# Kernel tuning notes

Hardware: AMD Instinct MI355X
Metric: run time of the kernel (lower is better)

The kernel has to match this reference:

```python
import jax, jax.numpy as jnp
import numpy as np

H = 128          # hidden_channels
K = 3            # TAGConv hops
NV, NS = 100000, 50000
EVV, ESS, EH, EIN = 1_000_000, 500_000, 500_000, 300_000


def setup_inputs() -> dict:
    key = jax.random.key(0)
    ks = iter(jax.random.split(key, 40))
    def rn(shape, s=0.05):
        return jax.random.normal(next(ks), shape, jnp.float32) * s
    def ri(shape, hi):
        return jax.random.randint(next(ks), shape, 0, hi, jnp.int32)
    return {
        "game_x": rn((NV, 5), 1.0),
        "state_x": rn((NS, 6), 1.0),
        "edge_index_v_v": ri((2, EVV), NV),
        "edge_type_v_v": ri((EVV,), 4),  # unused in forward (interface fidelity)
        "edge_index_history_v_s": jnp.stack([ri((EH,), NV), ri((EH,), NS)]),
        "edge_attr_history_v_s": rn((EH, 1), 1.0),
        "edge_index_in_v_s": jnp.stack([ri((EIN,), NV), ri((EIN,), NS)]),
        "edge_index_s_s": ri((2, ESS), NS),
        # TAGConv weights: (K+1) hop linears, shared bias
        "tag1_W": rn((K + 1, 5, H)), "tag1_b": rn((H,)),
        "tag2_W": rn((K + 1, 6, H)), "tag2_b": rn((H,)),
        # 7 SAGEConv layers stacked: gv[1:3]=0,1; sv[1:3]=2,3; in1=4; sv2=5,6
        "sage_Wl": rn((7, H, H)), "sage_bl": rn((7, H)), "sage_Wr": rn((7, H, H)),
        # GATConv (1 head, edge_dim=1)
        "gat_Wsrc": rn((H, H)), "gat_Wdst": rn((H, H)), "gat_We": rn((1, H)),
        "gat_asrc": rn((H,)), "gat_adst": rn((H,)), "gat_ae": rn((H,)), "gat_b": rn((H,)),
        # final MLP: single Linear(H, 1)
        "mlp_W": rn((H, 1)), "mlp_b": rn((1,)),
    }


def _seg_sum(x, idx, n):
    return jax.ops.segment_sum(x, idx, num_segments=n)


def tag_conv(x, edge_index, n, W, b):
    """TAGConv: out = sum_k lin_k(A_norm^k x) + b, gcn_norm w/o self loops."""
    src, dst = edge_index[0], edge_index[1]
    deg = _seg_sum(jnp.ones(src.shape, x.dtype), dst, n)
    dinv = jnp.where(deg > 0, jax.lax.rsqrt(jnp.maximum(deg, 1.0)), 0.0)
    norm = dinv[src] * dinv[dst]                      # [E]
    out = x @ W[0]
    h = x
    for k in range(1, W.shape[0]):
        h = _seg_sum(h[src] * norm[:, None], dst, n)  # one hop of normalized A
        out = out + h @ W[k]
    return out + b


def sage_conv(x_src, x_dst, edge_index, n_dst, Wl, bl, Wr):
    """SAGEConv(mean): lin_l(mean_j x_src[j]) + lin_r(x_dst)."""
    src, dst = edge_index[0], edge_index[1]
    s = _seg_sum(x_src[src], dst, n_dst)
    cnt = _seg_sum(jnp.ones(src.shape, x_src.dtype), dst, n_dst)
    mean = s / jnp.maximum(cnt, 1.0)[:, None]
    return mean @ Wl + bl + x_dst @ Wr


def gat_conv(x_src, x_dst, edge_index, edge_attr, n_dst,
             Wsrc, Wdst, We, asrc, adst, ae, b):
    """Bipartite GATConv, 1 head, edge features, no self loops."""
    src, dst = edge_index[0], edge_index[1]
    hs = x_src @ Wsrc                                  # [NV, H]
    hd = x_dst @ Wdst                                  # [NS, H]
    a = (hs @ asrc)[src] + (hd @ adst)[dst] + (edge_attr @ We) @ ae  # [E]
    a = jax.nn.leaky_relu(a, 0.2)
    m = jax.ops.segment_max(a, dst, num_segments=n_dst)
    e = jnp.exp(a - m[dst])                            # segment softmax
    denom = _seg_sum(e, dst, n_dst)
    alpha = e / jnp.maximum(denom, 1e-16)[dst]
    out = _seg_sum(alpha[:, None] * hs[src], dst, n_dst)
    return out + b


def reference(game_x, state_x, edge_index_v_v, edge_type_v_v,
              edge_index_history_v_s, edge_attr_history_v_s,
              edge_index_in_v_s, edge_index_s_s,
              tag1_W, tag1_b, tag2_W, tag2_b,
              sage_Wl, sage_bl, sage_Wr,
              gat_Wsrc, gat_Wdst, gat_We, gat_asrc, gat_adst, gat_ae, gat_b,
              mlp_W, mlp_b):
    relu = jax.nn.relu
    nv, ns = game_x.shape[0], state_x.shape[0]
    # game-vertex tower
    gx = relu(tag_conv(game_x, edge_index_v_v, nv, tag1_W, tag1_b))
    for i in range(2):
        gx = relu(sage_conv(gx, gx, edge_index_v_v, nv, sage_Wl[i], sage_bl[i], sage_Wr[i]))
    # state-vertex tower
    sx = relu(tag_conv(state_x, edge_index_s_s, ns, tag2_W, tag2_b))
    for i in range(2, 4):
        sx = relu(sage_conv(sx, sx, edge_index_s_s, ns, sage_Wl[i], sage_bl[i], sage_Wr[i]))
    # bipartite attention game -> state
    hist = relu(gat_conv(gx, sx, edge_index_history_v_s, edge_attr_history_v_s, ns,
                         gat_Wsrc, gat_Wdst, gat_We, gat_asrc, gat_adst, gat_ae, gat_b))
    in_x = relu(sage_conv(gx, hist, edge_index_in_v_s, ns, sage_Wl[4], sage_bl[4], sage_Wr[4]))
    # second state tower
    sx = in_x
    for i in range(5, 7):
        sx = relu(sage_conv(sx, sx, edge_index_s_s, ns, sage_Wl[i], sage_bl[i], sage_Wr[i]))
    return sx @ mlp_W + mlp_b                          # [NS, 1]
```

## Files before the change

### kernel.cpp

```cpp
#include <hip/hip_runtime.h>

#define H 128
typedef unsigned short u16;
typedef __attribute__((ext_vector_type(8))) short bf16x8;
typedef __attribute__((ext_vector_type(4))) float f32x4;


static inline int gridFor(long long work, int block, int cap = 16384){
  long long g = (work + block - 1) / block;
  if (g > cap) g = cap;
  if (g < 1) g = 1;
  return (int)g;
}

__device__ __forceinline__ float waveReduceSum(float v){
  #pragma unroll
  for(int off = 32; off > 0; off >>= 1) v += __shfl_down(v, off);
  return v;
}

__device__ __forceinline__ float bflo(unsigned v){ return __uint_as_float(v << 16); }
__device__ __forceinline__ float bfhi(unsigned v){ return __uint_as_float(v & 0xffff0000u); }
__device__ __forceinline__ u16 f2bf(float f){
  unsigned u = __float_as_uint(f);
  return (u16)((u + 0x7fffu + ((u >> 16) & 1u)) >> 16);
}
__device__ __forceinline__ unsigned pack2(float lo, float hi){
  return (unsigned)f2bf(lo) | ((unsigned)f2bf(hi) << 16);
}

#define BSHIFT 9
#define CH 2048

template<bool HAS_ATTR>
__global__ __launch_bounds__(256) void part_kernel(
    const int* __restrict__ src, const int* __restrict__ dst,
    const float* __restrict__ attr, int* __restrict__ bcur,
    int2* __restrict__ bpairs, float* __restrict__ battr, int E, int cap){
  __shared__ int hist[256];
  __shared__ int hscan[256];
  __shared__ int hbase[256];
  __shared__ int hcur[256];
  __shared__ int2 buf[CH];
  __shared__ float abuf[HAS_ATTR ? CH : 1];

  const int t = threadIdx.x;
  const int e0 = blockIdx.x * CH;
  const int cnt = min(CH, E - e0);

  hist[t] = 0; hcur[t] = 0;
  __syncthreads();

  #pragma unroll
  for(int j = 0; j < 8; j++){
    int i = e0 + j*256 + t;
    if(i - e0 < cnt) atomicAdd(&hist[dst[i] >> BSHIFT], 1);
  }
  __syncthreads();

  {
    int v = hist[t];
    int lane = t & 63, wid = t >> 6;
    int incl = v;
    #pragma unroll
    for(int off = 1; off < 64; off <<= 1){
      int u = __shfl_up(incl, off);
      if(lane >= off) incl += u;
    }
    __shared__ int ws4[4];
    if(lane == 63) ws4[wid] = incl;
    __syncthreads();
    int wofs = 0;
    for(int wj = 0; wj < wid; wj++) wofs += ws4[wj];
    hscan[t] = wofs + incl - v;
    hbase[t] = (v > 0) ? atomicAdd(&bcur[t], v) : 0;
  }
  __syncthreads();

  #pragma unroll
  for(int j = 0; j < 8; j++){
    int i = e0 + j*256 + t;
    if(i - e0 < cnt){
      int d = dst[i], s = src[i];
      int b = d >> BSHIFT;
      int lp = atomicAdd(&hcur[b], 1);
      int slot = hscan[b] + lp;
      buf[slot] = make_int2(d, s);
      if(HAS_ATTR) abuf[slot] = attr[i];
    }
  }
  __syncthreads();

  for(int u = t; u < cnt; u += 256){
    int2 pr = buf[u];
    int b = pr.x >> BSHIFT;
    int g = b * cap + hbase[b] + (u - hscan[b]);
    bpairs[g] = pr;
    if(HAS_ATTR) battr[g] = abuf[u];
  }
}

__global__ void bucket_scan(const int* __restrict__ bcur, int* __restrict__ bbase,
                            int* __restrict__ rp0, int* __restrict__ rp1,
                            int* __restrict__ rp2, int* __restrict__ rp3,
                            int n0, int n1, int n2, int n3){
  int g = blockIdx.x;
  int n = (g == 0) ? n0 : (g == 1) ? n1 : (g == 2) ? n2 : n3;
  int* rowp = (g == 0) ? rp0 : (g == 1) ? rp1 : (g == 2) ? rp2 : rp3;
  int NB = (n + 511) >> BSHIFT;
  int t = threadIdx.x;
  int v = (t < NB) ? bcur[g*256 + t] : 0;
  int lane = t & 63, wid = t >> 6;
  int incl = v;
  #pragma unroll
  for(int off = 1; off < 64; off <<= 1){
    int u = __shfl_up(incl, off);
    if(lane >= off) incl += u;
  }
  __shared__ int ws4[4];
  if(lane == 63) ws4[wid] = incl;
  __syncthreads();
  int wofs = 0;
  for(int wj = 0; wj < wid; wj++) wofs += ws4[wj];
  bbase[g*256 + t] = wofs + incl - v;
  if(t == 0) rowp[n] = ws4[0] + ws4[1] + ws4[2] + ws4[3];
}

template<bool HAS_ATTR, bool DINV>
__global__ __launch_bounds__(256) void build_kernel(
    const int2* __restrict__ bpairs, const float* __restrict__ battr,
    const int* __restrict__ bcur, const int* __restrict__ bbase,
    int* __restrict__ rowp, int* __restrict__ col, float* __restrict__ attrp,
    float* __restrict__ dinv, int cap, int n){
  __shared__ int hist[512];
  __shared__ int hcur[512];
  __shared__ int ws4[4];

  const int b = blockIdx.x;
  const int t = threadIdx.x;
  const int d0 = b << BSHIFT;
  const int dn = min(512, n - d0);
  const int cnt = bcur[b];
  const int base = bbase[b];
  const int2* ep = bpairs + (size_t)b * cap;

  hist[t] = 0; hist[t + 256] = 0;
  __syncthreads();
  for(int u = t; u < cnt; u += 256) atomicAdd(&hist[ep[u].x - d0], 1);
  __syncthreads();

  int a0 = hist[2*t], a1 = hist[2*t + 1];
  int s = a0 + a1;
  int lane = t & 63, wid = t >> 6;
  int incl = s;
  #pragma unroll
  for(int off = 1; off < 64; off <<= 1){
    int u = __shfl_up(incl, off);
    if(lane >= off) incl += u;
  }
  if(lane == 63) ws4[wid] = incl;
  __syncthreads();
  int wofs = 0;
  for(int wj = 0; wj < wid; wj++) wofs += ws4[wj];
  int excl = wofs + incl - s;
  __syncthreads();
  hcur[2*t] = excl; hcur[2*t + 1] = excl + a0;
  if(2*t < dn){
    rowp[d0 + 2*t] = base + excl;
    if(DINV) dinv[d0 + 2*t] = a0 > 0 ? rsqrtf((float)a0) : 0.f;
  }
  if(2*t + 1 < dn){
    rowp[d0 + 2*t + 1] = base + excl + a0;
    if(DINV) dinv[d0 + 2*t + 1] = a1 > 0 ? rsqrtf((float)a1) : 0.f;
  }
  __syncthreads();

  for(int u = t; u < cnt; u += 256){
    int2 pr = ep[u];
    int pos = base + atomicAdd(&hcur[pr.x - d0], 1);
    col[pos] = pr.y;
    if(HAS_ATTR) attrp[pos] = battr[(size_t)b * cap + u];
  }
}


__global__ void cvt_weights(const float* __restrict__ Wl, const float* __restrict__ Wr,
                            const float* __restrict__ Wsrc, u16* __restrict__ Wb){
  const int total = 15 * H * H;
  for(int t = blockIdx.x*blockDim.x + threadIdx.x; t < total; t += gridDim.x*blockDim.x){
    int mat = t >> 14, idx = t & 16383;
    int k = idx >> 7, colj = idx & 127;
    const float* srcp = (mat < 7) ? (Wl + ((size_t)mat << 14))
                       : (mat < 14) ? (Wr + ((size_t)(mat - 7) << 14))
                       : Wsrc;
    Wb[((size_t)mat << 14) + (size_t)colj*H + k] = f2bf(srcp[idx]);
  }
}

__global__ void mat_vec_row(const float* __restrict__ W, const float* __restrict__ a,
                            float* __restrict__ outv){
  int k = threadIdx.x;
  if(k < H){
    float s = 0.f;
    for(int j = 0; j < H; j++) s += W[(size_t)k*H + j] * a[j];
    outv[k] = s;
  }
}

__global__ void dot128(const float* __restrict__ a, const float* __restrict__ b,
                       float* __restrict__ o){
  int l = threadIdx.x;
  float acc = a[l]*b[l] + a[l+64]*b[l+64];
  acc = waveReduceSum(acc);
  if(l == 0) o[0] = acc;
}


template<int C>
__global__ void pack_rows(const float* __restrict__ x, const float* __restrict__ dinv,
                          float* __restrict__ xp, int N){
  for(int i = blockIdx.x*blockDim.x + threadIdx.x; i < N; i += gridDim.x*blockDim.x){
    #pragma unroll
    for(int k = 0; k < C; k++) xp[(size_t)i*8 + k] = x[(size_t)i*C + k];
    xp[(size_t)i*8 + 7] = dinv[i];
  }
}

template<int C>
__global__ void csr_tag_hop8(const int* __restrict__ rowp, const int* __restrict__ col,
                             const float* __restrict__ hin, float* __restrict__ hout, int N){
  for(int i = blockIdx.x*blockDim.x + threadIdx.x; i < N; i += gridDim.x*blockDim.x){
    int b = rowp[i], e = rowp[i+1];
    float dd = hin[(size_t)i*8 + 7];
    float acc0[C], acc1[C];
    #pragma unroll
    for(int k = 0; k < C; k++){ acc0[k] = 0.f; acc1[k] = 0.f; }
    int p = b;
    for(; p + 2 <= e; p += 2){
      const float* r0 = &hin[(size_t)col[p]   * 8];
      const float* r1 = &hin[(size_t)col[p+1] * 8];
      float w0 = r0[7] * dd, w1 = r1[7] * dd;
      #pragma unroll
      for(int k = 0; k < C; k++){
        acc0[k] += r0[k] * w0;
        acc1[k] += r1[k] * w1;
      }
    }
    if(p < e){
      const float* r0 = &hin[(size_t)col[p] * 8];
      float w0 = r0[7] * dd;
      #pragma unroll
      for(int k = 0; k < C; k++) acc0[k] += r0[k] * w0;
    }
    #pragma unroll
    for(int k = 0; k < C; k++) hout[(size_t)i*8 + k] = acc0[k] + acc1[k];
    hout[(size_t)i*8 + 7] = dd;
  }
}

template<int C>
__global__ __launch_bounds__(256) void tag_fuse(
    const float* __restrict__ x, const float* __restrict__ h1,
    const float* __restrict__ h2, const float* __restrict__ h3,
    const float* __restrict__ W, const float* __restrict__ bias,
    u16* __restrict__ out, int N){
  __shared__ float Ws[4*C*H];
  for(int u = threadIdx.x; u < 4*C*H; u += 256) Ws[u] = W[u];
  __syncthreads();
  const long long total = (long long)N * H;
  for(long long t = (long long)blockIdx.x*blockDim.x + threadIdx.x; t < total;
      t += (long long)gridDim.x*blockDim.x){
    int i = (int)(t >> 7), j = (int)(t & 127);
    const float* xr = x + (size_t)i*C;
    const float* r1 = h1 + (size_t)i*8;
    const float* r2 = h2 + (size_t)i*8;
    const float* r3 = h3 + (size_t)i*8;
    float acc = bias[j];
    #pragma unroll
    for(int k = 0; k < C; k++) acc += xr[k] * Ws[k*H + j];
    #pragma unroll
    for(int k = 0; k < C; k++) acc += r1[k] * Ws[(C + k)*H + j];
    #pragma unroll
    for(int k = 0; k < C; k++) acc += r2[k] * Ws[(2*C + k)*H + j];
    #pragma unroll
    for(int k = 0; k < C; k++) acc += r3[k] * Ws[(3*C + k)*H + j];
    out[t] = f2bf(fmaxf(acc, 0.f));
  }
}


__global__ __launch_bounds__(256) void sage_fused(
    const u16* __restrict__ G, const u16* __restrict__ X,
    const int* __restrict__ rowp, const int* __restrict__ col,
    const u16* __restrict__ WbR, const u16* __restrict__ WbL,
    const float* __restrict__ bl, u16* __restrict__ out, int N){
  __shared__ u16 Ws[H * H];

  const int t = threadIdx.x;
  const int lane = t & 63;
  const int wib = t >> 6;
  const int m0 = (blockIdx.x * 4 + wib) * 16;
  const int r16 = lane & 15;
  const int kg  = (lane >> 4) * 8;
  const bool active = (m0 < N);
  const int row = m0 + r16;

  for(int u = t; u < H*H/8; u += 256){
    bf16x8 v = *(const bf16x8*)&WbR[u*8];
    int c = u >> 4, kb = (u & 15) * 16;
    *(bf16x8*)((char*)Ws + c*256 + (kb ^ ((c & 7) << 4))) = v;
  }
  __syncthreads();

  f32x4 acc[8];
  #pragma unroll
  for(int tt = 0; tt < 8; tt++) acc[tt] = (f32x4){0.f,0.f,0.f,0.f};

  if(active){
    #pragma unroll
    for(int k0c = 0; k0c < 4; k0c++){
      int k0 = k0c * 32;
      bf16x8 af;
      if(row < N) af = *(const bf16x8*)&X[(size_t)row*H + k0 + kg];
      else        af = (bf16x8){0,0,0,0,0,0,0,0};
      #pragma unroll
      for(int tt = 0; tt < 8; tt++){
        int c = tt*16 + r16;
        int kb = (k0 + kg)*2;
        bf16x8 bf = *(const bf16x8*)((char*)Ws + c*256 + (kb ^ ((c & 7) << 4)));
        acc[tt] = __builtin_amdgcn_mfma_f32_16x16x32_bf16(af, bf, acc[tt], 0, 0, 0);
      }
    }
  }
  __syncthreads();

  for(int u = t; u < H*H/8; u += 256){
    bf16x8 v = *(const bf16x8*)&WbL[u*8];
    int c = u >> 4, kb = (u & 15) * 16;
    *(bf16x8*)((char*)Ws + c*256 + (kb ^ ((c & 7) << 4))) = v;
  }
  __syncthreads();

  if(active){
    float ag[4][8];
    #pragma unroll
    for(int kc = 0; kc < 4; kc++)
      #pragma unroll
      for(int j = 0; j < 8; j++) ag[kc][j] = 0.f;

    if(row < N){
      int b = rowp[row], e = rowp[row+1];
      for(int p = b; p < e; p++){
        int s = col[p];
        const u16* gr = &G[(size_t)s*H + kg];
        #pragma unroll
        for(int kc = 0; kc < 4; kc++){
          bf16x8 v = *(const bf16x8*)(gr + kc*32);
          const unsigned* vu = (const unsigned*)&v;
          #pragma unroll
          for(int q = 0; q < 4; q++){
            ag[kc][2*q]   += bflo(vu[q]);
            ag[kc][2*q+1] += bfhi(vu[q]);
          }
        }
      }
      float inv = 1.f / fmaxf((float)(e - b), 1.f);
      #pragma unroll
      for(int kc = 0; kc < 4; kc++)
        #pragma unroll
        for(int j = 0; j < 8; j++) ag[kc][j] *= inv;
    }

    #pragma unroll
    for(int kc = 0; kc < 4; kc++){
      unsigned uu[4];
      #pragma unroll
      for(int q = 0; q < 4; q++) uu[q] = pack2(ag[kc][2*q], ag[kc][2*q+1]);
      bf16x8 agb = *(bf16x8*)uu;
      int kb = (kc*32 + kg)*2;
      #pragma unroll
      for(int tt = 0; tt < 8; tt++){
        int c = tt*16 + r16;
        bf16x8 bf = *(const bf16x8*)((char*)Ws + c*256 + (kb ^ ((c & 7) << 4)));
        acc[tt] = __builtin_amdgcn_mfma_f32_16x16x32_bf16(agb, bf, acc[tt], 0, 0, 0);
      }
    }

    const int orow = m0 + (lane >> 4) * 4;
    #pragma unroll
    for(int tt = 0; tt < 8; tt++){
      int c = tt*16 + r16;
      float bb = bl[c];
      #pragma unroll
      for(int r = 0; r < 4; r++){
        if(orow + r < N){
          float v = fmaxf(acc[tt][r] + bb, 0.f);
          out[(size_t)(orow + r)*H + c] = f2bf(v);
        }
      }
    }
  }
}


__global__ __launch_bounds__(256) void gemm_mfma(
    const u16* __restrict__ x, const u16* __restrict__ Wb,
    u16* __restrict__ out, int N){
  __shared__ u16 Ws[H * H];
  const int t = threadIdx.x;
  for(int u = t; u < H*H/8; u += 256){
    bf16x8 v = *(const bf16x8*)&Wb[u*8];
    int c = u >> 4, kb = (u & 15) * 16;
    *(bf16x8*)((char*)Ws + c*256 + (kb ^ ((c & 7) << 4))) = v;
  }
  __syncthreads();

  const int lane = t & 63;
  const int wib = t >> 6;
  const int m0 = (blockIdx.x * 4 + wib) * 32;
  if(m0 >= N) return;
  const int r16 = lane & 15;
  const int kg = (lane >> 4) * 8;

  f32x4 acc[2][8];
  #pragma unroll
  for(int rt = 0; rt < 2; rt++)
    #pragma unroll
    for(int tt = 0; tt < 8; tt++) acc[rt][tt] = (f32x4){0.f,0.f,0.f,0.f};

  #pragma unroll
  for(int k0c = 0; k0c < 4; k0c++){
    int k0 = k0c * 32;
    bf16x8 af[2];
    #pragma unroll
    for(int rt = 0; rt < 2; rt++){
      int row = m0 + rt*16 + r16;
      if(row < N) af[rt] = *(const bf16x8*)&x[(size_t)row*H + k0 + kg];
      else        af[rt] = (bf16x8){0,0,0,0,0,0,0,0};
    }
    #pragma unroll
    for(int tt = 0; tt < 8; tt++){
      int c = tt*16 + r16;
      int kb = (k0 + kg)*2;
      bf16x8 bf = *(const bf16x8*)((char*)Ws + c*256 + (kb ^ ((c & 7) << 4)));
      acc[0][tt] = __builtin_amdgcn_mfma_f32_16x16x32_bf16(af[0], bf, acc[0][tt], 0, 0, 0);
      acc[1][tt] = __builtin_amdgcn_mfma_f32_16x16x32_bf16(af[1], bf, acc[1][tt], 0, 0, 0);
    }
  }

  #pragma unroll
  for(int rt = 0; rt < 2; rt++){
    const int orow = m0 + rt*16 + (lane >> 4) * 4;
    #pragma unroll
    for(int tt = 0; tt < 8; tt++){
      int c = tt*16 + r16;
      #pragma unroll
      for(int r = 0; r < 4; r++){
        if(orow + r < N)
          out[(size_t)(orow + r)*H + c] = f2bf(acc[rt][tt][r]);
      }
    }
  }
}


__global__ void rowdot_bf(const u16* __restrict__ x, const float* __restrict__ v,
                          float* __restrict__ out, int N){
  int lane = threadIdx.x & 63;
  int w = (blockIdx.x*blockDim.x + threadIdx.x) >> 6;
  int nw = (gridDim.x*blockDim.x) >> 6;
  for(int i = w; i < N; i += nw){
    unsigned u = *(const unsigned*)&x[(size_t)i*H + lane*2];
    float acc = bflo(u)*v[lane*2] + bfhi(u)*v[lane*2 + 1];
    acc = waveReduceSum(acc);
    if(lane == 0) out[i] = acc;
  }
}

__global__ void gat_fused(const int* __restrict__ rowp, const int* __restrict__ colv,
                          const float* __restrict__ attrp, const float* __restrict__ av,
                          const float* __restrict__ ad, const float* __restrict__ cptr,
                          const u16* __restrict__ hs, const float* __restrict__ bias,
                          u16* __restrict__ out, int N){
  const float c = cptr[0];
  int lane = threadIdx.x & 63;
  int w = (blockIdx.x*blockDim.x + threadIdx.x) >> 6;
  int nw = (gridDim.x*blockDim.x) >> 6;
  for(int i = w; i < N; i += nw){
    int b = rowp[i], e = rowp[i+1];
    float adi = ad[i];
    float accx0 = 0.f, accy0 = 0.f, accx1 = 0.f, accy1 = 0.f;
    float sume = 0.f;
    int p = b;
    for(; p + 2 <= e; p += 2){
      int s0 = colv[p], s1 = colv[p+1];
      float a0 = av[s0] + adi + attrp[p] * c;
      float a1 = av[s1] + adi + attrp[p+1] * c;
      a0 = a0 > 0.f ? a0 : 0.2f * a0;
      a1 = a1 > 0.f ? a1 : 0.2f * a1;
      float e0 = __expf(a0), e1 = __expf(a1);
      unsigned v0 = *(const unsigned*)&hs[(size_t)s0*H + lane*2];
      unsigned v1 = *(const unsigned*)&hs[(size_t)s1*H + lane*2];
      accx0 += e0 * bflo(v0); accy0 += e0 * bfhi(v0);
      accx1 += e1 * bflo(v1); accy1 += e1 * bfhi(v1);
      sume += e0 + e1;
    }
    if(p < e){
      int s0 = colv[p];
      float a0 = av[s0] + adi + attrp[p] * c;
      a0 = a0 > 0.f ? a0 : 0.2f * a0;
      float e0 = __expf(a0);
      unsigned v0 = *(const unsigned*)&hs[(size_t)s0*H + lane*2];
      accx0 += e0 * bflo(v0); accy0 += e0 * bfhi(v0);
      sume += e0;
    }
    float rd = 1.f / fmaxf(sume, 1e-16f);
    float ox = fmaxf((accx0 + accx1) * rd + bias[lane*2],     0.f);
    float oy = fmaxf((accy0 + accy1) * rd + bias[lane*2 + 1], 0.f);
    *(unsigned*)&out[(size_t)i*H + lane*2] = pack2(ox, oy);
  }
}

__global__ void mlp_out_bf(const u16* __restrict__ x, const float* __restrict__ W,
                           const float* __restrict__ b, float* __restrict__ out, int N){
  int lane = threadIdx.x & 63;
  int w = (blockIdx.x*blockDim.x + threadIdx.x) >> 6;
  int nw = (gridDim.x*blockDim.x) >> 6;
  for(int i = w; i < N; i += nw){
    unsigned u = *(const unsigned*)&x[(size_t)i*H + lane*2];
    float acc = bflo(u)*W[lane*2] + bfhi(u)*W[lane*2 + 1];
    acc = waveReduceSum(acc);
    if(lane == 0) out[i] = acc + b[0];
  }
}


extern "C" void kernel_launch(void* const* d_in, const int* in_sizes, int n_in,
                              void* d_out, int out_size, void* d_ws, size_t ws_size,
                              hipStream_t stream) {
  const float* game_x  = (const float*)d_in[0];
  const float* state_x = (const float*)d_in[1];
  const int*   e_vv    = (const int*)d_in[2];
  const int*   e_hist  = (const int*)d_in[4];
  const float* attr_h  = (const float*)d_in[5];
  const int*   e_in    = (const int*)d_in[6];
  const int*   e_ss    = (const int*)d_in[7];
  const float* tag1_W  = (const float*)d_in[8];
  const float* tag1_b  = (const float*)d_in[9];
  const float* tag2_W  = (const float*)d_in[10];
  const float* tag2_b  = (const float*)d_in[11];
  const float* sage_Wl = (const float*)d_in[12];
  const float* sage_bl = (const float*)d_in[13];
  const float* sage_Wr = (const float*)d_in[14];
  const float* gat_Wsrc= (const float*)d_in[15];
  const float* gat_Wdst= (const float*)d_in[16];
  const float* gat_We  = (const float*)d_in[17];
  const float* gat_asrc= (const float*)d_in[18];
  const float* gat_adst= (const float*)d_in[19];
  const float* gat_ae  = (const float*)d_in[20];
  const float* gat_b   = (const float*)d_in[21];
  const float* mlp_W   = (const float*)d_in[22];
  const float* mlp_b   = (const float*)d_in[23];
  float* out = (float*)d_out;

  const int NV  = in_sizes[0] / 5;
  const int NS  = in_sizes[1] / 6;
  const int EVV = in_sizes[2] / 2;
  const int EH  = in_sizes[4] / 2;
  const int EIN = in_sizes[6] / 2;
  const int ESS = in_sizes[7] / 2;

  const int* vv_src = e_vv;   const int* vv_dst = e_vv + EVV;
  const int* eh_src = e_hist; const int* eh_dst = e_hist + EH;
  const int* in_src = e_in;   const int* in_dst = e_in + EIN;
  const int* ss_src = e_ss;   const int* ss_dst = e_ss + ESS;

  const int NBv = (NV + 511) >> BSHIFT;
  const int NBs = (NS + 511) >> BSHIFT;
  const int capvv = (EVV / NBv) * 3 / 2 + 64;
  const int capss = (ESS / NBs) * 3 / 2 + 64;
  const int capeh = (EH  / NBs) * 3 / 2 + 64;
  const int capin = (EIN / NBs) * 3 / 2 + 64;

  char* wp = (char*)d_ws;
  auto alloc = [&](size_t bytes) -> void* {
    void* p = (void*)wp;
    wp += (bytes + 511) & ~size_t(511);
    return p;
  };
  u16* V0 = (u16*)alloc((size_t)NV*H*2);
  u16* V1 = (u16*)alloc((size_t)NV*H*2);
  u16* S0 = (u16*)alloc((size_t)NS*H*2);
  u16* S1 = (u16*)alloc((size_t)NS*H*2);
  u16* Wb = (u16*)alloc((size_t)15*H*H*2);
  float* dinv_v = (float*)alloc((size_t)NV*4);
  float* dinv_s = (float*)alloc((size_t)NS*4);
  float* av   = (float*)alloc((size_t)NV*4);
  float* ad   = (float*)alloc((size_t)NS*4);
  float* xp5  = (float*)alloc((size_t)NV*8*4);
  float* h5a  = (float*)alloc((size_t)NV*8*4);
  float* h5b  = (float*)alloc((size_t)NV*8*4);
  float* h5c  = (float*)alloc((size_t)NV*8*4);
  float* xp6  = (float*)alloc((size_t)NS*8*4);
  float* h6a  = (float*)alloc((size_t)NS*8*4);
  float* h6b  = (float*)alloc((size_t)NS*8*4);
  float* h6c  = (float*)alloc((size_t)NS*8*4);
  float* wvec = (float*)alloc(H*4);
  float* cbuf = (float*)alloc(4);
  int* vv_rowp = (int*)alloc((size_t)(NV+1)*4);
  int* vv_col  = (int*)alloc((size_t)EVV*4);
  int* ss_rowp = (int*)alloc((size_t)(NS+1)*4);
  int* ss_col  = (int*)alloc((size_t)ESS*4);
  int* eh_rowp = (int*)alloc((size_t)(NS+1)*4);
  int* eh_col  = (int*)alloc((size_t)EH*4);
  float* eh_attr = (float*)alloc((size_t)EH*4);
  int* in_rowp = (int*)alloc((size_t)(NS+1)*4);
  int* in_col  = (int*)alloc((size_t)EIN*4);
  int2* vv_bp = (int2*)alloc((size_t)NBv*capvv*8);
  int2* ss_bp = (int2*)alloc((size_t)NBs*capss*8);
  int2* eh_bp = (int2*)alloc((size_t)NBs*capeh*8);
  int2* in_bp = (int2*)alloc((size_t)NBs*capin*8);
  float* eh_ba = (float*)alloc((size_t)NBs*capeh*4);
  int* bcur  = (int*)alloc(4*256*4);
  int* bbase = (int*)alloc(4*256*4);
  (void)ws_size; (void)n_in; (void)out_size;

  const int B = 256;
  #define GRID1(n) gridFor((long long)(n), B, 8192), B, 0, stream
  #define GRIDW(e) gridFor((long long)(e) * 64, B, 16384), B, 0, stream
  #define GEMM(n)  ((n) + 63) / 64, 256, 0, stream

  hipMemsetAsync(bcur, 0, 4*256*4, stream);
  part_kernel<false><<<(EVV + CH - 1)/CH, 256, 0, stream>>>(
      vv_src, vv_dst, nullptr, bcur + 0,   vv_bp, nullptr, EVV, capvv);
  part_kernel<false><<<(ESS + CH - 1)/CH, 256, 0, stream>>>(
      ss_src, ss_dst, nullptr, bcur + 256, ss_bp, nullptr, ESS, capss);
  part_kernel<true ><<<(EH  + CH - 1)/CH, 256, 0, stream>>>(
      eh_src, eh_dst, attr_h,  bcur + 512, eh_bp, eh_ba,   EH,  capeh);
  part_kernel<false><<<(EIN + CH - 1)/CH, 256, 0, stream>>>(
      in_src, in_dst, nullptr, bcur + 768, in_bp, nullptr, EIN, capin);
  bucket_scan<<<4, 256, 0, stream>>>(bcur, bbase, vv_rowp, ss_rowp, eh_rowp, in_rowp,
                                     NV, NS, NS, NS);
  build_kernel<false,true ><<<NBv, 256, 0, stream>>>(
      vv_bp, nullptr, bcur + 0,   bbase + 0,   vv_rowp, vv_col, nullptr, dinv_v, capvv, NV);
  build_kernel<false,true ><<<NBs, 256, 0, stream>>>(
      ss_bp, nullptr, bcur + 256, bbase + 256, ss_rowp, ss_col, nullptr, dinv_s, capss, NS);
  build_kernel<true ,false><<<NBs, 256, 0, stream>>>(
      eh_bp, eh_ba,   bcur + 512, bbase + 512, eh_rowp, eh_col, eh_attr, nullptr, capeh, NS);
  build_kernel<false,false><<<NBs, 256, 0, stream>>>(
      in_bp, nullptr, bcur + 768, bbase + 768, in_rowp, in_col, nullptr, nullptr, capin, NS);

  cvt_weights<<<GRID1(15*H*H)>>>(sage_Wl, sage_Wr, gat_Wsrc, Wb);
  mat_vec_row<<<1, 128, 0, stream>>>(gat_Wdst, gat_adst, wvec);
  dot128<<<1, 64, 0, stream>>>(gat_We, gat_ae, cbuf);

  #define WBL(l) (Wb + ((size_t)(l) << 14))
  #define WBR(l) (Wb + ((size_t)(7 + (l)) << 14))

  pack_rows<5><<<GRID1(NV)>>>(game_x, dinv_v, xp5, NV);
  csr_tag_hop8<5><<<GRID1(NV)>>>(vv_rowp, vv_col, xp5, h5a, NV);
  csr_tag_hop8<5><<<GRID1(NV)>>>(vv_rowp, vv_col, h5a, h5b, NV);
  csr_tag_hop8<5><<<GRID1(NV)>>>(vv_rowp, vv_col, h5b, h5c, NV);
  tag_fuse<5><<<GRID1((long long)NV*H)>>>(game_x, h5a, h5b, h5c, tag1_W, tag1_b, V0, NV);

  sage_fused<<<GEMM(NV)>>>(V0, V0, vv_rowp, vv_col, WBR(0), WBL(0),
                           sage_bl + 0*H, V1, NV);
  sage_fused<<<GEMM(NV)>>>(V1, V1, vv_rowp, vv_col, WBR(1), WBL(1),
                           sage_bl + 1*H, V0, NV);

  pack_rows<6><<<GRID1(NS)>>>(state_x, dinv_s, xp6, NS);
  csr_tag_hop8<6><<<GRID1(NS)>>>(ss_rowp, ss_col, xp6, h6a, NS);
  csr_tag_hop8<6><<<GRID1(NS)>>>(ss_rowp, ss_col, h6a, h6b, NS);
  csr_tag_hop8<6><<<GRID1(NS)>>>(ss_rowp, ss_col, h6b, h6c, NS);
  tag_fuse<6><<<GRID1((long long)NS*H)>>>(state_x, h6a, h6b, h6c, tag2_W, tag2_b, S0, NS);

  sage_fused<<<GEMM(NS)>>>(S0, S0, ss_rowp, ss_col, WBR(2), WBL(2),
                           sage_bl + 2*H, S1, NS);
  sage_fused<<<GEMM(NS)>>>(S1, S1, ss_rowp, ss_col, WBR(3), WBL(3),
                           sage_bl + 3*H, S0, NS);

  gemm_mfma<<<((NV + 127)/128), 256, 0, stream>>>(V0, Wb + ((size_t)14 << 14), V1, NV);
  rowdot_bf<<<GRIDW(NV)>>>(V1, gat_asrc, av, NV);
  rowdot_bf<<<GRIDW(NS)>>>(S0, wvec, ad, NS);
  gat_fused<<<GRIDW(NS)>>>(eh_rowp, eh_col, eh_attr, av, ad, cbuf, V1, gat_b, S1, NS);

  sage_fused<<<GEMM(NS)>>>(V0, S1, in_rowp, in_col, WBR(4), WBL(4),
                           sage_bl + 4*H, S0, NS);

  sage_fused<<<GEMM(NS)>>>(S0, S0, ss_rowp, ss_col, WBR(5), WBL(5),
                           sage_bl + 5*H, S1, NS);
  sage_fused<<<GEMM(NS)>>>(S1, S1, ss_rowp, ss_col, WBR(6), WBL(6),
                           sage_bl + 6*H, S0, NS);

  mlp_out_bf<<<GRIDW(NS)>>>(S0, mlp_W, mlp_b, out, NS);

  #undef GRID1
  #undef GRIDW
  #undef GEMM
  #undef WBL
  #undef WBR
}
```

Baseline: 908.8 us.

## Gather SAGE neighbor rows wave-cooperatively per row and transpose via LDS

The mean-aggregation gather in the fused SAGE kernel changes from each lane walking one row's neighbor list with 16-byte loads to the whole wave processing one destination row at a time. Each lane loads 4 bytes of each neighbor row, giving coalesced 256-byte row reads, and the inner loop is unrolled 8 neighbors deep to keep more loads in flight. The results are staged in a small LDS buffer and read back in the MFMA A-fragment layout. This removes load imbalance from uneven degrees across the 16 rows in a wave, at the cost of serializing the 16 rows and extra LDS traffic.

```diff
diff --git a/kernel.cpp b/kernel.cpp
--- a/kernel.cpp
+++ b/kernel.cpp
@@ -295,6 +295,7 @@
     const u16* __restrict__ WbR, const u16* __restrict__ WbL,
     const float* __restrict__ bl, u16* __restrict__ out, int N){
   __shared__ u16 Ws[H * H];
+  __shared__ unsigned Tr[4][16][68];
 
   const int t = threadIdx.x;
   const int lane = t & 63;
@@ -303,7 +304,6 @@
   const int r16 = lane & 15;
   const int kg  = (lane >> 4) * 8;
   const bool active = (m0 < N);
-  const int row = m0 + r16;
 
   for(int u = t; u < H*H/8; u += 256){
     bf16x8 v = *(const bf16x8*)&WbR[u*8];
@@ -317,6 +317,7 @@
   for(int tt = 0; tt < 8; tt++) acc[tt] = (f32x4){0.f,0.f,0.f,0.f};
 
   if(active){
+    const int row = m0 + r16;
     #pragma unroll
     for(int k0c = 0; k0c < 4; k0c++){
       int k0 = k0c * 32;
@@ -342,41 +343,38 @@
   __syncthreads();
 
   if(active){
-    float ag[4][8];
-    #pragma unroll
-    for(int kc = 0; kc < 4; kc++)
-      #pragma unroll
-      for(int j = 0; j < 8; j++) ag[kc][j] = 0.f;
-
-    if(row < N){
-      int b = rowp[row], e = rowp[row+1];
-      for(int p = b; p < e; p++){
-        int s = col[p];
-        const u16* gr = &G[(size_t)s*H + kg];
+    for(int r = 0; r < 16; r++){
+      int row = m0 + r;
+      unsigned packed = 0;
+      if(row < N){
+        int b = rowp[row], e = rowp[row+1];
+        float xs[8], ys[8];
         #pragma unroll
-        for(int kc = 0; kc < 4; kc++){
-          bf16x8 v = *(const bf16x8*)(gr + kc*32);
-          const unsigned* vu = (const unsigned*)&v;
+        for(int j = 0; j < 8; j++){ xs[j] = 0.f; ys[j] = 0.f; }
+        int p = b;
+        for(; p + 8 <= e; p += 8){
+          unsigned v[8];
           #pragma unroll
-          for(int q = 0; q < 4; q++){
-            ag[kc][2*q]   += bflo(vu[q]);
-            ag[kc][2*q+1] += bfhi(vu[q]);
-          }
+          for(int j = 0; j < 8; j++)
+            v[j] = *(const unsigned*)&G[(size_t)col[p + j]*H + lane*2];
+          #pragma unroll
+          for(int j = 0; j < 8; j++){ xs[j] += bflo(v[j]); ys[j] += bfhi(v[j]); }
         }
+        for(; p < e; p++){
+          unsigned v = *(const unsigned*)&G[(size_t)col[p]*H + lane*2];
+          xs[0] += bflo(v); ys[0] += bfhi(v);
+        }
+        float sx = (xs[0]+xs[1])+(xs[2]+xs[3])+((xs[4]+xs[5])+(xs[6]+xs[7]));
+        float sy = (ys[0]+ys[1])+(ys[2]+ys[3])+((ys[4]+ys[5])+(ys[6]+ys[7]));
+        float inv = 1.f / fmaxf((float)(e - b), 1.f);
+        packed = pack2(sx*inv, sy*inv);
       }
-      float inv = 1.f / fmaxf((float)(e - b), 1.f);
-      #pragma unroll
-      for(int kc = 0; kc < 4; kc++)
-        #pragma unroll
-        for(int j = 0; j < 8; j++) ag[kc][j] *= inv;
+      Tr[wib][r][lane] = packed;
     }
 
     #pragma unroll
     for(int kc = 0; kc < 4; kc++){
-      unsigned uu[4];
-      #pragma unroll
-      for(int q = 0; q < 4; q++) uu[q] = pack2(ag[kc][2*q], ag[kc][2*q+1]);
-      bf16x8 agb = *(bf16x8*)uu;
+      bf16x8 agb = *(const bf16x8*)&Tr[wib][r16][(lane >> 4)*4 + kc*16];
       int kb = (kc*32 + kg)*2;
       #pragma unroll
       for(int tt = 0; tt < 8; tt++){
```

Measured after the change: 1.323 ms. 45.6% more time.

## Group SAGE rows by in-degree via permutation to balance wave gather loops

Applied to the files above, without the earlier changes.

Adds a deg_scatter kernel that builds, per graph, a permutation of destination rows bucketed by in-degree (capped at 63). Each 4096-row chunk groups its rows by degree and claims positions with a global atomic, so rows of equal degree sit together only inside a chunk. sage_fused now processes rows in permuted order, so the 16 rows in a wave have similar neighbour counts and less lane divergence in the gather loop. It also unrolls the neighbour loop by two to keep more loads in flight. The cost is scattered output writes and X reads, and extra indirection through perm.

```diff
diff --git a/kernel.cpp b/kernel.cpp
--- a/kernel.cpp
+++ b/kernel.cpp
@@ -183,6 +183,32 @@
   }
 }
 
+__global__ __launch_bounds__(256) void deg_scatter(
+    const int* __restrict__ rowp, int* __restrict__ gcur,
+    int* __restrict__ perm, int n){
+  __shared__ int lh[64], lbase[64], lcur[64];
+  const int t = threadIdx.x;
+  const int base = blockIdx.x * 4096;
+  if(base >= n) return;
+  const int cnt = min(4096, n - base);
+  if(t < 64){ lh[t] = 0; lcur[t] = 0; }
+  __syncthreads();
+  for(int i = t; i < cnt; i += 256){
+    int r = base + i;
+    int d = min(rowp[r+1] - rowp[r], 63);
+    atomicAdd(&lh[d], 1);
+  }
+  __syncthreads();
+  if(t < 64) lbase[t] = (lh[t] > 0) ? atomicAdd(gcur, lh[t]) : 0;
+  __syncthreads();
+  for(int i = t; i < cnt; i += 256){
+    int r = base + i;
+    int d = min(rowp[r+1] - rowp[r], 63);
+    int lp = atomicAdd(&lcur[d], 1);
+    perm[lbase[d] + lp] = r;
+  }
+}
+
 
 __global__ void cvt_weights(const float* __restrict__ Wl, const float* __restrict__ Wr,
                             const float* __restrict__ Wsrc, u16* __restrict__ Wb){
@@ -292,6 +318,7 @@
 __global__ __launch_bounds__(256) void sage_fused(
     const u16* __restrict__ G, const u16* __restrict__ X,
     const int* __restrict__ rowp, const int* __restrict__ col,
+    const int* __restrict__ perm,
     const u16* __restrict__ WbR, const u16* __restrict__ WbL,
     const float* __restrict__ bl, u16* __restrict__ out, int N){
   __shared__ u16 Ws[H * H];
@@ -303,7 +330,7 @@
   const int r16 = lane & 15;
   const int kg  = (lane >> 4) * 8;
   const bool active = (m0 < N);
-  const int row = m0 + r16;
+  const int arow = (m0 + r16 < N) ? perm[m0 + r16] : -1;
 
   for(int u = t; u < H*H/8; u += 256){
     bf16x8 v = *(const bf16x8*)&WbR[u*8];
@@ -321,8 +348,8 @@
     for(int k0c = 0; k0c < 4; k0c++){
       int k0 = k0c * 32;
       bf16x8 af;
-      if(row < N) af = *(const bf16x8*)&X[(size_t)row*H + k0 + kg];
-      else        af = (bf16x8){0,0,0,0,0,0,0,0};
+      if(arow >= 0) af = *(const bf16x8*)&X[(size_t)arow*H + k0 + kg];
+      else          af = (bf16x8){0,0,0,0,0,0,0,0};
       #pragma unroll
       for(int tt = 0; tt < 8; tt++){
         int c = tt*16 + r16;
@@ -348,19 +375,36 @@
       #pragma unroll
       for(int j = 0; j < 8; j++) ag[kc][j] = 0.f;
 
-    if(row < N){
-      int b = rowp[row], e = rowp[row+1];
-      for(int p = b; p < e; p++){
-        int s = col[p];
-        const u16* gr = &G[(size_t)s*H + kg];
+    if(arow >= 0){
+      int b = rowp[arow], e = rowp[arow+1];
+      int p = b;
+      for(; p + 2 <= e; p += 2){
+        int s0 = col[p], s1 = col[p+1];
+        const u16* g0 = &G[(size_t)s0*H + kg];
+        const u16* g1 = &G[(size_t)s1*H + kg];
         #pragma unroll
         for(int kc = 0; kc < 4; kc++){
-          bf16x8 v = *(const bf16x8*)(gr + kc*32);
-          const unsigned* vu = (const unsigned*)&v;
+          bf16x8 v0 = *(const bf16x8*)(g0 + kc*32);
+          bf16x8 v1 = *(const bf16x8*)(g1 + kc*32);
+          const unsigned* u0 = (const unsigned*)&v0;
+          const unsigned* u1 = (const unsigned*)&v1;
           #pragma unroll
           for(int q = 0; q < 4; q++){
-            ag[kc][2*q]   += bflo(vu[q]);
-            ag[kc][2*q+1] += bfhi(vu[q]);
+            ag[kc][2*q]   += bflo(u0[q]) + bflo(u1[q]);
+            ag[kc][2*q+1] += bfhi(u0[q]) + bfhi(u1[q]);
+          }
+        }
+      }
+      if(p < e){
+        const u16* g0 = &G[(size_t)col[p]*H + kg];
+        #pragma unroll
+        for(int kc = 0; kc < 4; kc++){
+          bf16x8 v0 = *(const bf16x8*)(g0 + kc*32);
+          const unsigned* u0 = (const unsigned*)&v0;
+          #pragma unroll
+          for(int q = 0; q < 4; q++){
+            ag[kc][2*q]   += bflo(u0[q]);
+            ag[kc][2*q+1] += bfhi(u0[q]);
           }
         }
       }
@@ -386,16 +430,21 @@
       }
     }
 
-    const int orow = m0 + (lane >> 4) * 4;
+    int op[4];
+    #pragma unroll
+    for(int r = 0; r < 4; r++){
+      int oidx = m0 + (lane >> 4)*4 + r;
+      op[r] = (oidx < N) ? perm[oidx] : -1;
+    }
     #pragma unroll
     for(int tt = 0; tt < 8; tt++){
       int c = tt*16 + r16;
       float bb = bl[c];
       #pragma unroll
       for(int r = 0; r < 4; r++){
-        if(orow + r < N){
+        if(op[r] >= 0){
           float v = fmaxf(acc[tt][r] + bb, 0.f);
-          out[(size_t)(orow + r)*H + c] = f2bf(v);
+          out[(size_t)op[r]*H + c] = f2bf(v);
         }
       }
     }
@@ -616,6 +665,9 @@
   float* eh_attr = (float*)alloc((size_t)EH*4);
   int* in_rowp = (int*)alloc((size_t)(NS+1)*4);
   int* in_col  = (int*)alloc((size_t)EIN*4);
+  int* perm_vv = (int*)alloc((size_t)NV*4);
+  int* perm_ss = (int*)alloc((size_t)NS*4);
+  int* perm_in = (int*)alloc((size_t)NS*4);
   int2* vv_bp = (int2*)alloc((size_t)NBv*capvv*8);
   int2* ss_bp = (int2*)alloc((size_t)NBs*capss*8);
   int2* eh_bp = (int2*)alloc((size_t)NBs*capeh*8);
@@ -623,6 +675,7 @@
   float* eh_ba = (float*)alloc((size_t)NBs*capeh*4);
   int* bcur  = (int*)alloc(4*256*4);
   int* bbase = (int*)alloc(4*256*4);
+  int* pcur  = (int*)alloc(3*4);
   (void)ws_size; (void)n_in; (void)out_size;
 
   const int B = 256;
@@ -631,6 +684,7 @@
   #define GEMM(n)  ((n) + 63) / 64, 256, 0, stream
 
   hipMemsetAsync(bcur, 0, 4*256*4, stream);
+  hipMemsetAsync(pcur, 0, 3*4, stream);
   part_kernel<false><<<(EVV + CH - 1)/CH, 256, 0, stream>>>(
       vv_src, vv_dst, nullptr, bcur + 0,   vv_bp, nullptr, EVV, capvv);
   part_kernel<false><<<(ESS + CH - 1)/CH, 256, 0, stream>>>(
@@ -650,6 +704,10 @@
   build_kernel<false,false><<<NBs, 256, 0, stream>>>(
       in_bp, nullptr, bcur + 768, bbase + 768, in_rowp, in_col, nullptr, nullptr, capin, NS);
 
+  deg_scatter<<<(NV + 4095)/4096, 256, 0, stream>>>(vv_rowp, pcur + 0, perm_vv, NV);
+  deg_scatter<<<(NS + 4095)/4096, 256, 0, stream>>>(ss_rowp, pcur + 1, perm_ss, NS);
+  deg_scatter<<<(NS + 4095)/4096, 256, 0, stream>>>(in_rowp, pcur + 2, perm_in, NS);
+
   cvt_weights<<<GRID1(15*H*H)>>>(sage_Wl, sage_Wr, gat_Wsrc, Wb);
   mat_vec_row<<<1, 128, 0, stream>>>(gat_Wdst, gat_adst, wvec);
   dot128<<<1, 64, 0, stream>>>(gat_We, gat_ae, cbuf);
@@ -663,9 +721,9 @@
   csr_tag_hop8<5><<<GRID1(NV)>>>(vv_rowp, vv_col, h5b, h5c, NV);
   tag_fuse<5><<<GRID1((long long)NV*H)>>>(game_x, h5a, h5b, h5c, tag1_W, tag1_b, V0, NV);
 
-  sage_fused<<<GEMM(NV)>>>(V0, V0, vv_rowp, vv_col, WBR(0), WBL(0),
+  sage_fused<<<GEMM(NV)>>>(V0, V0, vv_rowp, vv_col, perm_vv, WBR(0), WBL(0),
                            sage_bl + 0*H, V1, NV);
-  sage_fused<<<GEMM(NV)>>>(V1, V1, vv_rowp, vv_col, WBR(1), WBL(1),
+  sage_fused<<<GEMM(NV)>>>(V1, V1, vv_rowp, vv_col, perm_vv, WBR(1), WBL(1),
                            sage_bl + 1*H, V0, NV);
 
   pack_rows<6><<<GRID1(NS)>>>(state_x, dinv_s, xp6, NS);
@@ -674,9 +732,9 @@
   csr_tag_hop8<6><<<GRID1(NS)>>>(ss_rowp, ss_col, h6b, h6c, NS);
   tag_fuse<6><<<GRID1((long long)NS*H)>>>(state_x, h6a, h6b, h6c, tag2_W, tag2_b, S0, NS);
 
-  sage_fused<<<GEMM(NS)>>>(S0, S0, ss_rowp, ss_col, WBR(2), WBL(2),
+  sage_fused<<<GEMM(NS)>>>(S0, S0, ss_rowp, ss_col, perm_ss, WBR(2), WBL(2),
                            sage_bl + 2*H, S1, NS);
-  sage_fused<<<GEMM(NS)>>>(S1, S1, ss_rowp, ss_col, WBR(3), WBL(3),
+  sage_fused<<<GEMM(NS)>>>(S1, S1, ss_rowp, ss_col, perm_ss, WBR(3), WBL(3),
                            sage_bl + 3*H, S0, NS);
 
   gemm_mfma<<<((NV + 127)/128), 256, 0, stream>>>(V0, Wb + ((size_t)14 << 14), V1, NV);
@@ -684,12 +742,12 @@
   rowdot_bf<<<GRIDW(NS)>>>(S0, wvec, ad, NS);
   gat_fused<<<GRIDW(NS)>>>(eh_rowp, eh_col, eh_attr, av, ad, cbuf, V1, gat_b, S1, NS);
 
-  sage_fused<<<GEMM(NS)>>>(V0, S1, in_rowp, in_col, WBR(4), WBL(4),
+  sage_fused<<<GEMM(NS)>>>(V0, S1, in_rowp, in_col, perm_in, WBR(4), WBL(4),
                            sage_bl + 4*H, S0, NS);
 
-  sage_fused<<<GEMM(NS)>>>(S0, S0, ss_rowp, ss_col, WBR(5), WBL(5),
+  sage_fused<<<GEMM(NS)>>>(S0, S0, ss_rowp, ss_col, perm_ss, WBR(5), WBL(5),
                            sage_bl + 5*H, S1, NS);
-  sage_fused<<<GEMM(NS)>>>(S1, S1, ss_rowp, ss_col, WBR(6), WBL(6),
+  sage_fused<<<GEMM(NS)>>>(S1, S1, ss_rowp, ss_col, perm_ss, WBR(6), WBL(6),
                            sage_bl + 6*H, S0, NS);
 
   mlp_out_bf<<<GRIDW(NS)>>>(S0, mlp_W, mlp_b, out, NS);
```

After: 901.6 us. Within noise of the previous version (-0.8%).
